# Optimization experiments

Measured on AMD Instinct MI355X. Metric: run time of the kernel, lower is better.

## Reference

```python
import jax, jax.numpy as jnp
import numpy as np

B, T, E = 2, 1024, 256   # batch, context, input_emb_size
D = 64                   # query_key_emb_size
DV = 64                  # output_ebm_size


def setup_inputs() -> dict:
    key = jax.random.key(0)
    ks = jax.random.split(key, 12)
    s_in = 1.0 / np.sqrt(E)
    s_2d = 1.0 / np.sqrt(2 * D)
    s_d = 1.0 / np.sqrt(D)
    return {
        "x":  jax.random.normal(ks[0], (B, T, E), dtype=jnp.float32),
        "Wq": jax.random.uniform(ks[1], (E, D), jnp.float32, -s_in, s_in),
        "bq": jax.random.uniform(ks[2], (D,), jnp.float32, -s_in, s_in),
        "Wk": jax.random.uniform(ks[3], (E, D), jnp.float32, -s_in, s_in),
        "bk": jax.random.uniform(ks[4], (D,), jnp.float32, -s_in, s_in),
        "Wv": jax.random.uniform(ks[5], (E, DV), jnp.float32, -s_in, s_in),
        "bv": jax.random.uniform(ks[6], (DV,), jnp.float32, -s_in, s_in),
        "W1": jax.random.uniform(ks[7], (2 * D, D), jnp.float32, -s_2d, s_2d),
        "b1": jax.random.uniform(ks[8], (D,), jnp.float32, -s_2d, s_2d),
        "W2": jax.random.uniform(ks[9], (D, 1), jnp.float32, -s_d, s_d),
        "b2": jax.random.uniform(ks[10], (1,), jnp.float32, -s_d, s_d),
    }


def reference(x, Wq, bq, Wk, bk, Wv, bv, W1, b1, W2, b2):
    # projections (dropout_p = 0 -> dropouts are identity)
    q = jax.nn.relu(x @ Wq + bq)        # [B,T,D]  (activation applied pre-pairing)
    k = jax.nn.relu(x @ Wk + bk)        # [B,T,D]
    v = x @ Wv + bv                     # [B,T,DV]
    t = x.shape[-2]
    d = q.shape[-1]
    # lnr1(concat[q_i, k_j]) == q_i @ W1[:D] + k_j @ W1[D:] + b1 -- avoids the
    # O(T^2 * 2D) concat tensor the torch code materializes via repeat_interleave.
    qp = q @ W1[:d]                     # [B,T,D]
    kp = k @ W1[d:]                     # [B,T,D]
    h = jax.nn.relu(qp[:, :, None, :] + kp[:, None, :, :] + b1)   # [B,T,T,D]
    scores = jnp.einsum('bqkd,d->bqk', h, W2[:, 0]) + b2[0]       # [B,T,T]
    causal = jnp.tril(jnp.ones((t, t), dtype=bool))
    scores = jnp.where(causal, scores, -jnp.inf)
    weights = jax.nn.softmax(scores, axis=-1)                     # [B,T,T]
    out = jnp.einsum('bqk,bkv->bqv', weights, v)                  # [B,T,DV]
    return out
```

## Files before the change

kernel.cpp:

```cpp
#include <hip/hip_runtime.h>

#define B_SZ   2
#define T_CTX  1024
#define E_IN   256
#define D_QK   64
#define DV_OUT 64
#define NROWS  (B_SZ * T_CTX)
#define RPB    4
#define QT     4
#define CH     128
#define NTILE  256
#define BLKS_PER_B 1152


__global__ __launch_bounds__(256) void proj_kernel(
    const float* __restrict__ x,
    const float* __restrict__ Wq, const float* __restrict__ bq,
    const float* __restrict__ Wk, const float* __restrict__ bk,
    const float* __restrict__ Wv, const float* __restrict__ bv,
    const float* __restrict__ W1, const float* __restrict__ b1,
    float* __restrict__ qpb, float* __restrict__ kpt, float* __restrict__ v,
    float* __restrict__ outacc, float* __restrict__ lacc)
{
    __shared__ float xs[RPB * E_IN];
    __shared__ float qs[RPB * D_QK];
    __shared__ float ks[RPB * D_QK];
    __shared__ float kps[RPB * D_QK];

    const int row0 = blockIdx.x * RPB;
    const int t    = threadIdx.x;

    outacc[(size_t)row0 * DV_OUT + t] = 0.f;
    if (t < RPB) lacc[row0 + t] = 0.f;

    *(float4*)&xs[4 * t] = *(const float4*)&x[(size_t)row0 * E_IN + 4 * t];
    __syncthreads();

    const int d = t & 63;
    const int r = t >> 6;
    const float* xrow = &xs[r * E_IN];

    float aq0 = 0.f, aq1 = 0.f, ak0 = 0.f, ak1 = 0.f, av0 = 0.f, av1 = 0.f;
    #pragma unroll 8
    for (int e = 0; e < E_IN; e += 2) {
        float x0 = xrow[e], x1 = xrow[e + 1];
        aq0 += x0 * Wq[(e)     * D_QK   + d];
        aq1 += x1 * Wq[(e + 1) * D_QK   + d];
        ak0 += x0 * Wk[(e)     * D_QK   + d];
        ak1 += x1 * Wk[(e + 1) * D_QK   + d];
        av0 += x0 * Wv[(e)     * DV_OUT + d];
        av1 += x1 * Wv[(e + 1) * DV_OUT + d];
    }
    qs[r * D_QK + d] = fmaxf(aq0 + aq1 + bq[d], 0.f);
    ks[r * D_QK + d] = fmaxf(ak0 + ak1 + bk[d], 0.f);
    v[(size_t)(row0 + r) * DV_OUT + d] = av0 + av1 + bv[d];
    __syncthreads();

    const float* qrow = &qs[r * D_QK];
    const float* krow = &ks[r * D_QK];
    float ap0 = 0.f, ap1 = 0.f, bp0 = 0.f, bp1 = 0.f;
    #pragma unroll 8
    for (int e = 0; e < D_QK; e += 2) {
        ap0 += qrow[e]     * W1[(e)            * D_QK + d];
        ap1 += qrow[e + 1] * W1[(e + 1)        * D_QK + d];
        bp0 += krow[e]     * W1[(D_QK + e)     * D_QK + d];
        bp1 += krow[e + 1] * W1[(D_QK + e + 1) * D_QK + d];
    }
    qpb[(size_t)(row0 + r) * D_QK + d] = ap0 + ap1 + b1[d];
    kps[r * D_QK + d] = bp0 + bp1;
    __syncthreads();

    if (t < D_QK) {
        float4 kq = make_float4(kps[0 * D_QK + t], kps[1 * D_QK + t],
                                kps[2 * D_QK + t], kps[3 * D_QK + t]);
        *(float4*)&kpt[(size_t)t * NROWS + row0] = kq;
    }
}

__global__ __launch_bounds__(128) void attn_kernel(
    const float* __restrict__ qpb, const float* __restrict__ kpt,
    const float* __restrict__ v,
    const float* __restrict__ W2, const float* __restrict__ b2,
    float* __restrict__ outacc, float* __restrict__ lacc)
{
    __shared__ float qqT[D_QK][QT];
    __shared__ float w2s[D_QK];
    __shared__ float pT[CH][QT];
    __shared__ float redl[2][QT];
    __shared__ float part[2][QT][DV_OUT];

    int u = blockIdx.x;
    int b = 0;
    if (u >= BLKS_PER_B) { b = 1; u -= BLKS_PER_B; }
    int g = 0;
    while (u >= 16 * (g + 1) * (g + 2)) ++g;
    const int loc   = u - 16 * g * (g + 1);
    const int tidx  = loc / (g + 1);
    const int chunk = loc - tidx * (g + 1);
    const int tile  = 32 * g + tidx;
    const int i0    = tile * QT;
    const int jc    = chunk * CH;

    const int t    = threadIdx.x;
    const int lane = t & 63;
    const int wv   = t >> 6;
    const size_t base = (size_t)b * T_CTX;

    #pragma unroll
    for (int k = t; k < QT * D_QK; k += 128) {
        const int q = k >> 6, d = k & 63;
        qqT[d][q] = qpb[(base + i0 + q) * D_QK + d];
    }
    if (t < D_QK) w2s[t] = W2[t];
    __syncthreads();

    const float bias2 = b2[0];
    const int j = jc + t;
    const float* kb = kpt + base + j;

    float acc[QT];
    #pragma unroll
    for (int q = 0; q < QT; ++q) acc[q] = 0.f;

    #pragma unroll 8
    for (int dd = 0; dd < D_QK; ++dd) {
        float kv  = kb[(size_t)dd * NROWS];
        float4 qa = *(const float4*)&qqT[dd][0];
        float wd  = w2s[dd];
        acc[0] += fmaxf(qa.x + kv, 0.f) * wd;
        acc[1] += fmaxf(qa.y + kv, 0.f) * wd;
        acc[2] += fmaxf(qa.z + kv, 0.f) * wd;
        acc[3] += fmaxf(qa.w + kv, 0.f) * wd;
    }

    const int rel = j - i0;
    float p[QT];
    #pragma unroll
    for (int q = 0; q < QT; ++q)
        p[q] = (rel <= q) ? __expf(bias2 + acc[q]) : 0.f;
    *(float4*)&pT[t][0] = make_float4(p[0], p[1], p[2], p[3]);

    #pragma unroll
    for (int q = 0; q < QT; ++q) {
        float lq = p[q];
        #pragma unroll
        for (int o = 32; o > 0; o >>= 1) lq += __shfl_xor(lq, o, 64);
        if (lane == 0) redl[wv][q] = lq;
    }
    __syncthreads();
    if (t < QT) atomicAdd(&lacc[base + i0 + t], redl[0][t] + redl[1][t]);

    const int half = lane >> 5;
    const int dp   = (lane & 31) * 2;
    float2 av2[QT];
    #pragma unroll
    for (int q = 0; q < QT; ++q) av2[q] = make_float2(0.f, 0.f);

    const float* vb = v + (base + jc + 64 * wv) * DV_OUT + dp;
    #pragma unroll 8
    for (int jj = 0; jj < 64; jj += 2) {
        const int jl = 64 * wv + jj + half;
        float2 vv2 = *(const float2*)(vb + (size_t)(jj + half) * DV_OUT);
        float4 pj  = *(const float4*)&pT[jl][0];
        av2[0].x += pj.x * vv2.x; av2[0].y += pj.x * vv2.y;
        av2[1].x += pj.y * vv2.x; av2[1].y += pj.y * vv2.y;
        av2[2].x += pj.z * vv2.x; av2[2].y += pj.z * vv2.y;
        av2[3].x += pj.w * vv2.x; av2[3].y += pj.w * vv2.y;
    }
    #pragma unroll
    for (int q = 0; q < QT; ++q) {
        av2[q].x += __shfl_xor(av2[q].x, 32, 64);
        av2[q].y += __shfl_xor(av2[q].y, 32, 64);
    }
    if (half == 0) {
        #pragma unroll
        for (int q = 0; q < QT; ++q)
            *(float2*)&part[wv][q][dp] = av2[q];
    }
    __syncthreads();

    #pragma unroll
    for (int k = t; k < QT * DV_OUT; k += 128) {
        const int q = k >> 6, dv = k & 63;
        atomicAdd(&outacc[(base + i0 + q) * DV_OUT + dv],
                  part[0][q][dv] + part[1][q][dv]);
    }
}

__global__ __launch_bounds__(512) void finalize_kernel(
    const float* __restrict__ outacc, const float* __restrict__ lacc,
    float* __restrict__ out)
{
    const size_t idx = (size_t)blockIdx.x * 512 + threadIdx.x;
    out[idx] = outacc[idx] / lacc[idx >> 6];
}

extern "C" void kernel_launch(void* const* d_in, const int* in_sizes, int n_in,
                              void* d_out, int out_size, void* d_ws, size_t ws_size,
                              hipStream_t stream) {
    const float* x  = (const float*)d_in[0];
    const float* Wq = (const float*)d_in[1];
    const float* bq = (const float*)d_in[2];
    const float* Wk = (const float*)d_in[3];
    const float* bk = (const float*)d_in[4];
    const float* Wv = (const float*)d_in[5];
    const float* bv = (const float*)d_in[6];
    const float* W1 = (const float*)d_in[7];
    const float* b1 = (const float*)d_in[8];
    const float* W2 = (const float*)d_in[9];
    const float* b2 = (const float*)d_in[10];
    float* out = (float*)d_out;

    float* ws     = (float*)d_ws;
    float* qpb    = ws;
    float* kpt    = ws + (size_t)NROWS * D_QK;
    float* vv     = ws + (size_t)2 * NROWS * D_QK;
    float* outacc = ws + (size_t)3 * NROWS * D_QK;
    float* lacc   = ws + (size_t)4 * NROWS * D_QK;

    proj_kernel<<<NROWS / RPB, 256, 0, stream>>>(x, Wq, bq, Wk, bk, Wv, bv,
                                                 W1, b1, qpb, kpt, vv,
                                                 outacc, lacc);
    attn_kernel<<<B_SZ * BLKS_PER_B, CH, 0, stream>>>(qpb, kpt, vv, W2, b2,
                                                      outacc, lacc);
    finalize_kernel<<<(NROWS * DV_OUT) / 512, 512, 0, stream>>>(outacc, lacc,
                                                                out);
}
```

Measured before the change: 40.16 us.

## Remap block indices to keep batch and key chunks local to each XCD

Both the projection and attention kernels now decode blockIdx so that blocks landing on the same XCD (blockIdx mod 8) work on the same batch and a paired set of key chunks (kk and 7-kk). Each XCD therefore reads and writes a consistent subset of K/V rows, qpb tiles and outacc rows. The aim is to improve L2 locality on MI355X's per-XCD caches and to balance the causal triangular work across XCDs. The scheme relies on round-robin dispatch of blocks to XCDs and on hardcoded grid sizes.

```diff
diff --git a/kernel.cpp b/kernel.cpp
--- a/kernel.cpp
+++ b/kernel.cpp
@@ -9,8 +9,6 @@
 #define RPB    4
 #define QT     4
 #define CH     128
-#define NTILE  256
-#define BLKS_PER_B 1152
 
 
 __global__ __launch_bounds__(256) void proj_kernel(
@@ -27,8 +25,16 @@
     __shared__ float ks[RPB * D_QK];
     __shared__ float kps[RPB * D_QK];
 
-    const int row0 = blockIdx.x * RPB;
-    const int t    = threadIdx.x;
+    const int P   = blockIdx.x;
+    const int xcd = P & 7;
+    const int slt = P >> 3;
+    const int bb  = xcd >> 2;
+    const int kk  = xcd & 3;
+    const int row0 = (slt < 32)
+        ? bb * T_CTX + kk * 128 + slt * 4
+        : bb * T_CTX + (7 - kk) * 128 + (slt - 32) * 4;
+
+    const int t = threadIdx.x;
 
     outacc[(size_t)row0 * DV_OUT + t] = 0.f;
     if (t < RPB) lacc[row0 + t] = 0.f;
@@ -89,17 +95,17 @@
     __shared__ float redl[2][QT];
     __shared__ float part[2][QT][DV_OUT];
 
-    int u = blockIdx.x;
-    int b = 0;
-    if (u >= BLKS_PER_B) { b = 1; u -= BLKS_PER_B; }
-    int g = 0;
-    while (u >= 16 * (g + 1) * (g + 2)) ++g;
-    const int loc   = u - 16 * g * (g + 1);
-    const int tidx  = loc / (g + 1);
-    const int chunk = loc - tidx * (g + 1);
-    const int tile  = 32 * g + tidx;
-    const int i0    = tile * QT;
-    const int jc    = chunk * CH;
+    const int P   = blockIdx.x;
+    const int xcd = P & 7;
+    const int slt = P >> 3;
+    const int b   = xcd >> 2;
+    const int kk  = xcd & 3;
+    const int n1  = 256 - 32 * kk;
+    int tile, chunk;
+    if (slt < n1) { chunk = kk;     tile = 32 * kk + slt; }
+    else          { chunk = 7 - kk; tile = 32 * (7 - kk) + (slt - n1); }
+    const int i0 = tile * QT;
+    const int jc = chunk * CH;
 
     const int t    = threadIdx.x;
     const int lane = t & 63;
@@ -107,8 +113,8 @@
     const size_t base = (size_t)b * T_CTX;
 
     #pragma unroll
-    for (int k = t; k < QT * D_QK; k += 128) {
-        const int q = k >> 6, d = k & 63;
+    for (int kq = t; kq < QT * D_QK; kq += 128) {
+        const int q = kq >> 6, d = kq & 63;
         qqT[d][q] = qpb[(base + i0 + q) * D_QK + d];
     }
     if (t < D_QK) w2s[t] = W2[t];
@@ -180,8 +186,8 @@
     __syncthreads();
 
     #pragma unroll
-    for (int k = t; k < QT * DV_OUT; k += 128) {
-        const int q = k >> 6, dv = k & 63;
+    for (int kq = t; kq < QT * DV_OUT; kq += 128) {
+        const int q = kq >> 6, dv = kq & 63;
         atomicAdd(&outacc[(base + i0 + q) * DV_OUT + dv],
                   part[0][q][dv] + part[1][q][dv]);
     }
@@ -221,8 +227,7 @@
     proj_kernel<<<NROWS / RPB, 256, 0, stream>>>(x, Wq, bq, Wk, bk, Wv, bv,
                                                  W1, b1, qpb, kpt, vv,
                                                  outacc, lacc);
-    attn_kernel<<<B_SZ * BLKS_PER_B, CH, 0, stream>>>(qpb, kpt, vv, W2, b2,
-                                                      outacc, lacc);
+    attn_kernel<<<2304, CH, 0, stream>>>(qpb, kpt, vv, W2, b2, outacc, lacc);
     finalize_kernel<<<(NROWS * DV_OUT) / 512, 512, 0, stream>>>(outacc, lacc,
                                                                 out);
 }
```

After: 36.62 us, median of 3. 8.8% less time.
